# Performance work log

Hardware: AMD Instinct MI355X
Metric: run time of the kernel (lower is better)

The kernel has to match this reference:

```python
import jax, jax.numpy as jnp
import numpy as np


def _conv1x1(x, w, b):
    # x: (B, C, H, W), w: (O, C), b: (O,) -> (B, O, H, W)
    return jnp.einsum('bchw,oc->bohw', x, w) + b[None, :, None, None]


def setup_inputs() -> dict:
    key = jax.random.key(0)
    ks = jax.random.split(key, 9)
    C, Cb = 256, 128
    B, H, W = 4, 64, 64
    s_in = 1.0 / np.sqrt(C)   # kaiming-uniform-ish scale for 1x1 convs
    s_bn = 1.0 / np.sqrt(Cb)
    return {
        'x': jax.random.normal(ks[0], (B, C, H, W), dtype=jnp.float32),
        'theta_w': jax.random.uniform(ks[1], (Cb, C), jnp.float32, -s_in, s_in),
        'theta_b': jax.random.uniform(ks[2], (Cb,), jnp.float32, -s_in, s_in),
        'phi_w': jax.random.uniform(ks[3], (Cb, C), jnp.float32, -s_in, s_in),
        'phi_b': jax.random.uniform(ks[4], (Cb,), jnp.float32, -s_in, s_in),
        'g_w': jax.random.uniform(ks[5], (Cb, C), jnp.float32, -s_in, s_in),
        'g_b': jax.random.uniform(ks[6], (Cb,), jnp.float32, -s_in, s_in),
        'W_w': jax.random.uniform(ks[7], (C, Cb), jnp.float32, -s_bn, s_bn),
        'W_b': jax.random.uniform(ks[8], (C,), jnp.float32, -s_bn, s_bn),
    }


def reference(x, theta_w, theta_b, phi_w, phi_b, g_w, g_b, W_w, W_b):
    B, C, H, Wd = x.shape
    Cb = theta_w.shape[0]
    # NOTE: the original uses raw torch.reshape (row-major), NOT transpose,
    # so (B, Cb, H, W) -> (B, H*W, Cb) scrambles channel/spatial layout.
    # We replicate that exactly with jnp.reshape.
    theta = _conv1x1(x, theta_w, theta_b).reshape(B, -1, Cb)   # (B, N, Cb)
    phi = _conv1x1(x, phi_w, phi_b).reshape(B, Cb, -1)         # (B, Cb, N)
    g = _conv1x1(x, g_w, g_b).reshape(B, -1, Cb)               # (B, N, Cb)
    scores = jnp.einsum('bnc,bcm->bnm', theta, phi)            # (B, N, N)
    attn = jax.nn.softmax(scores, axis=1)                      # softmax over dim=1 (unusual axis)
    y = jnp.einsum('bnm,bmc->bnc', attn, g)                    # (B, N, Cb)
    y = y.reshape(B, -1, H, Wd)                                # raw reshape back to (B, Cb, H, W)
    w = _conv1x1(y, W_w, W_b)                                  # (B, C, H, W)
    return w + x
```

## Files before the change

### kernel.cpp

```cpp
#include <hip/hip_runtime.h>
#include <math.h>


constexpr int CI = 256;
constexpr int CB = 128;
constexpr int HWD = 4096;
constexpr int NBATCH = 4;
constexpr int NN_ = 4096;
constexpr size_t U1 = (size_t)NBATCH * NN_ * CB;
constexpr size_t U_THETA = 0;
constexpr size_t U_PHIT  = U1;
constexpr size_t U_G     = 2 * U1;
constexpr size_t U_GT    = 3 * U1;
constexpr size_t U_Y     = 4 * U1;
constexpr size_t U_XT    = 4 * U1;
constexpr size_t U_WCAT  = 8 * U1;
constexpr size_t U_WW    = 8 * U1 + 98304;
constexpr size_t F_D     = (8 * U1 + 131072) / 2;

typedef short v8s __attribute__((ext_vector_type(8)));
typedef unsigned short u8s __attribute__((ext_vector_type(8)));
typedef float v4f __attribute__((ext_vector_type(4)));
#define MFMA16(a, b, c) __builtin_amdgcn_mfma_f32_16x16x32_bf16(a, b, c, 0, 0, 0)

__device__ __forceinline__ unsigned short f2bf(float f) {
    union { float f; unsigned u; } v; v.f = f;
    unsigned r = v.u + 0x7fff + ((v.u >> 16) & 1);
    return (unsigned short)(r >> 16);
}
__device__ __forceinline__ float bf2f(unsigned short s) {
    union { unsigned u; float f; } v; v.u = (unsigned)s << 16;
    return v.f;
}

__global__ __launch_bounds__(256) void k0_xpose(
    const float* __restrict__ x, unsigned short* __restrict__ xT)
{
    __shared__ unsigned short T[64 * 72];
    const int t = threadIdx.x;
    const int hw0 = blockIdx.x * 64, c0 = blockIdx.y * 64, b = blockIdx.z;
    const float* xb = x + (size_t)b * CI * HWD;
    const int rr = t >> 4, cc = t & 15;
    #pragma unroll
    for (int pass = 0; pass < 4; pass++) {
        float4 f = *(const float4*)&xb[(size_t)(c0 + pass * 16 + rr) * HWD + hw0 + cc * 4];
        T[(cc * 4 + 0) * 72 + pass * 16 + rr] = f2bf(f.x);
        T[(cc * 4 + 1) * 72 + pass * 16 + rr] = f2bf(f.y);
        T[(cc * 4 + 2) * 72 + pass * 16 + rr] = f2bf(f.z);
        T[(cc * 4 + 3) * 72 + pass * 16 + rr] = f2bf(f.w);
    }
    __syncthreads();
    const int row = t >> 2, cs = (t & 3) * 16;
    unsigned short* dst = xT + (size_t)b * NN_ * CI;
    #pragma unroll
    for (int h = 0; h < 2; h++)
        *(u8s*)&dst[(size_t)(hw0 + row) * CI + c0 + cs + h * 8] =
            *(const u8s*)&T[row * 72 + cs + h * 8];
}

__global__ __launch_bounds__(256) void k0_weights(
    const float* __restrict__ tw, const float* __restrict__ pw,
    const float* __restrict__ gw, const float* __restrict__ Ww,
    unsigned short* __restrict__ wcat, unsigned short* __restrict__ wwB)
{
    int e = (blockIdx.x * 256 + threadIdx.x) * 4;
    const float* src; unsigned short* dst;
    if (e < 32768)       { src = tw + e;          dst = wcat + e; }
    else if (e < 65536)  { src = pw + (e - 32768); dst = wcat + e; }
    else if (e < 98304)  { src = gw + (e - 65536); dst = wcat + e; }
    else                 { src = Ww + (e - 98304); dst = wwB + (e - 98304); }
    float4 f = *(const float4*)src;
    ushort4 u;
    u.x = f2bf(f.x); u.y = f2bf(f.y); u.z = f2bf(f.z); u.w = f2bf(f.w);
    *(ushort4*)dst = u;
}

__global__ __launch_bounds__(256, 2) void k1_mfma(
    const unsigned short* __restrict__ xT, const unsigned short* __restrict__ wcat,
    const float* __restrict__ tb, const float* __restrict__ pb,
    const float* __restrict__ gb,
    unsigned short* __restrict__ thetaB, unsigned short* __restrict__ phiTB,
    unsigned short* __restrict__ gB)
{
    __shared__ unsigned short T[64 * 72];
    const int t = threadIdx.x;
    const int lane = t & 63, w = t >> 6;
    const int ln = lane & 15, quad = lane >> 4;
    const int hw0 = blockIdx.x * 64, j0 = blockIdx.y * 64, b = blockIdx.z;
    const int matId = j0 >> 7, jl0 = j0 & 127;
    const float* bvec = (matId == 0) ? tb : (matId == 1) ? pb : gb;
    const unsigned short* xb = xT + (size_t)b * NN_ * CI;

    v8s aw[8];
    #pragma unroll
    for (int kt = 0; kt < 8; kt++)
        aw[kt] = *(const v8s*)&wcat[(size_t)(j0 + w * 16 + ln) * CI + kt * 32 + quad * 8];

    v4f s[4] = {};
    v8s bx[4], bxn[4];
    #pragma unroll
    for (int mt = 0; mt < 4; mt++)
        bx[mt] = *(const v8s*)&xb[(size_t)(hw0 + mt * 16 + ln) * CI + quad * 8];
    #pragma unroll
    for (int kt = 0; kt < 8; kt++) {
        if (kt < 7) {
            #pragma unroll
            for (int mt = 0; mt < 4; mt++)
                bxn[mt] = *(const v8s*)&xb[(size_t)(hw0 + mt * 16 + ln) * CI + (kt + 1) * 32 + quad * 8];
        }
        #pragma unroll
        for (int mt = 0; mt < 4; mt++)
            s[mt] = MFMA16(aw[kt], bx[mt], s[mt]);
        #pragma unroll
        for (int mt = 0; mt < 4; mt++) bx[mt] = bxn[mt];
    }

    float bias[4];
    #pragma unroll
    for (int r = 0; r < 4; r++) bias[r] = bvec[jl0 + w * 16 + quad * 4 + r];

    if (matId != 1) {
        unsigned short* dst = ((matId == 0) ? thetaB : gB) + (size_t)b * CB * HWD;
        #pragma unroll
        for (int mt = 0; mt < 4; mt++)
            #pragma unroll
            for (int r = 0; r < 4; r++)
                dst[(size_t)(jl0 + w * 16 + quad * 4 + r) * HWD + hw0 + mt * 16 + ln] =
                    f2bf(s[mt][r] + bias[r]);
    } else {
        #pragma unroll
        for (int mt = 0; mt < 4; mt++) {
            ushort4 pk;
            pk.x = f2bf(s[mt][0] + bias[0]);
            pk.y = f2bf(s[mt][1] + bias[1]);
            pk.z = f2bf(s[mt][2] + bias[2]);
            pk.w = f2bf(s[mt][3] + bias[3]);
            *(ushort4*)&T[(mt * 16 + ln) * 72 + w * 16 + quad * 4] = pk;
        }
        __syncthreads();
        unsigned short* dst = phiTB + (size_t)b * NN_ * CB;
        const int row = t >> 2, cs = (t & 3) * 16;
        #pragma unroll
        for (int h = 0; h < 2; h++)
            *(u8s*)&dst[(size_t)(hw0 + row) * CB + jl0 + cs + h * 8] =
                *(const u8s*)&T[row * 72 + cs + h * 8];
    }
}

__global__ __launch_bounds__(256, 4) void k2_colsum(
    const unsigned short* __restrict__ thetaB,
    const unsigned short* __restrict__ phiTB,
    float* __restrict__ Dout)
{
    __shared__ float part[4][64];
    const int t = threadIdx.x;
    const int lane = t & 63, w = t >> 6;
    const int ln = lane & 15, quad = lane >> 4;
    const int m0 = blockIdx.x * 64, q = blockIdx.y, b = blockIdx.z;
    const unsigned short* th = thetaB + (size_t)b * NN_ * CB;
    const unsigned short* ph = phiTB + (size_t)b * NN_ * CB;

    v8s bf[4][4];
    #pragma unroll
    for (int mt = 0; mt < 4; mt++)
        #pragma unroll
        for (int kt = 0; kt < 4; kt++)
            bf[mt][kt] = *(const v8s*)&ph[(size_t)(m0 + mt * 16 + ln) * CB + kt * 32 + quad * 8];

    float dsum[4] = {0.f, 0.f, 0.f, 0.f};
    const int nBeg = q * 1024 + w * 16, nEnd = q * 1024 + 1024;
    v8s af[4], afn[4];
    #pragma unroll
    for (int kt = 0; kt < 4; kt++)
        af[kt] = *(const v8s*)&th[(size_t)(nBeg + ln) * CB + kt * 32 + quad * 8];
    for (int n0 = nBeg; n0 < nEnd; n0 += 64) {
        int nn = (n0 + 64 < nEnd) ? n0 + 64 : nBeg;
        #pragma unroll
        for (int kt = 0; kt < 4; kt++)
            afn[kt] = *(const v8s*)&th[(size_t)(nn + ln) * CB + kt * 32 + quad * 8];
        v4f s[4] = {};
        #pragma unroll
        for (int mt = 0; mt < 4; mt++)
            #pragma unroll
            for (int kt = 0; kt < 4; kt++)
                s[mt] = MFMA16(af[kt], bf[mt][kt], s[mt]);
        #pragma unroll
        for (int mt = 0; mt < 4; mt++)
            #pragma unroll
            for (int r = 0; r < 4; r++)
                dsum[mt] += __expf(s[mt][r]);
        #pragma unroll
        for (int kt = 0; kt < 4; kt++) af[kt] = afn[kt];
    }
    #pragma unroll
    for (int mt = 0; mt < 4; mt++) {
        float v = dsum[mt];
        v += __shfl_xor(v, 16);
        v += __shfl_xor(v, 32);
        dsum[mt] = v;
    }
    if (quad == 0) {
        #pragma unroll
        for (int mt = 0; mt < 4; mt++) part[w][mt * 16 + ln] = dsum[mt];
    }
    __syncthreads();
    if (t < 64) {
        float v = part[0][t] + part[1][t] + part[2][t] + part[3][t];
        Dout[((size_t)q * NBATCH + b) * NN_ + m0 + t] = v;
    }
}

__global__ __launch_bounds__(256) void k1b_transpose_scale_g(
    const unsigned short* __restrict__ gB, const float* __restrict__ D,
    unsigned short* __restrict__ gTB)
{
    const int t = threadIdx.x;
    const int m0 = blockIdx.x * 32;
    const int c0 = blockIdx.y * 64;
    const int b  = blockIdx.z;
    const unsigned short* src = gB + (size_t)b * CB * HWD;
    unsigned short* dst = gTB + (size_t)b * CB * HWD;
    const int c = c0 + (t & 63);
    const int mseg = (t >> 6) * 8;
    u8s pack;
    #pragma unroll
    for (int j = 0; j < 8; j++) {
        int m = m0 + mseg + j;
        float d = D[((size_t)0 * NBATCH + b) * NN_ + m]
                + D[((size_t)1 * NBATCH + b) * NN_ + m]
                + D[((size_t)2 * NBATCH + b) * NN_ + m]
                + D[((size_t)3 * NBATCH + b) * NN_ + m];
        float r = 1.0f / d;
        pack[j] = f2bf(bf2f(src[(size_t)m * CB + c]) * r);
    }
    *(u8s*)&dst[(size_t)c * HWD + m0 + mseg] = pack;
}

__global__ __launch_bounds__(256, 4) void k3_attn(
    const unsigned short* __restrict__ thetaB,
    const unsigned short* __restrict__ phiTB,
    const unsigned short* __restrict__ gTB,
    unsigned short* __restrict__ Y)
{
    __shared__ unsigned short Lphi[64 * 136];
    __shared__ unsigned short Pl[64][72];
    const int t = threadIdx.x;
    const int lane = t & 63, w = t >> 6;
    const int ln = lane & 15, quad = lane >> 4;
    const int rowS = t >> 4, colS = t & 15;
    const int n0 = blockIdx.x * 64, q = blockIdx.y, b = blockIdx.z;
    const unsigned short* th = thetaB + (size_t)b * NN_ * CB;
    const unsigned short* ph = phiTB + (size_t)b * NN_ * CB;
    const unsigned short* gT = gTB + (size_t)b * CB * HWD;

    v8s ath[4];
    #pragma unroll
    for (int kt = 0; kt < 4; kt++)
        ath[kt] = *(const v8s*)&th[(size_t)(n0 + w * 16 + ln) * CB + kt * 32 + quad * 8];

    const int mBeg = q * 1024, mEnd = mBeg + 1024;
    #pragma unroll
    for (int pass = 0; pass < 4; pass++) {
        v8s v = *(const v8s*)&ph[(size_t)(mBeg + pass * 16 + rowS) * CB + colS * 8];
        *(v8s*)&Lphi[(pass * 16 + rowS) * 136 + colS * 8] = v;
    }
    __syncthreads();

    v4f yacc[2][4] = {};
    for (int m0 = mBeg; m0 < mEnd; m0 += 64) {
        int mN = (m0 + 64 < mEnd) ? m0 + 64 : mBeg;
        v8s preg[4];
        #pragma unroll
        for (int pass = 0; pass < 4; pass++)
            preg[pass] = *(const v8s*)&ph[(size_t)(mN + pass * 16 + rowS) * CB + colS * 8];
        v8s gfrag[2][2];
        #pragma unroll
        for (int ct = 0; ct < 2; ct++)
            #pragma unroll
            for (int kt2 = 0; kt2 < 2; kt2++)
                gfrag[ct][kt2] = *(const v8s*)&gT[(size_t)(w * 32 + ct * 16 + ln) * HWD + m0 + kt2 * 32 + quad * 8];
        v4f s[4] = {};
        #pragma unroll
        for (int mt = 0; mt < 4; mt++)
            #pragma unroll
            for (int kt = 0; kt < 4; kt++) {
                v8s bphi = *(const v8s*)&Lphi[(mt * 16 + ln) * 136 + kt * 32 + quad * 8];
                s[mt] = MFMA16(ath[kt], bphi, s[mt]);
            }
        float pv[4][4];
        #pragma unroll
        for (int mt = 0; mt < 4; mt++)
            #pragma unroll
            for (int r = 0; r < 4; r++)
                pv[mt][r] = __expf(s[mt][r]);
        __syncthreads();
        #pragma unroll
        for (int mt = 0; mt < 4; mt++)
            #pragma unroll
            for (int r = 0; r < 4; r++)
                Pl[w * 16 + quad * 4 + r][mt * 16 + ln] = f2bf(pv[mt][r]);
        #pragma unroll
        for (int pass = 0; pass < 4; pass++)
            *(v8s*)&Lphi[(pass * 16 + rowS) * 136 + colS * 8] = preg[pass];
        __syncthreads();
        #pragma unroll
        for (int ct = 0; ct < 2; ct++)
            #pragma unroll
            for (int kt2 = 0; kt2 < 2; kt2++)
                #pragma unroll
                for (int nt = 0; nt < 4; nt++) {
                    v8s ap = *(const v8s*)&Pl[nt * 16 + ln][kt2 * 32 + quad * 8];
                    yacc[ct][nt] = MFMA16(ap, gfrag[ct][kt2], yacc[ct][nt]);
                }
    }
    unsigned short* yp = Y + ((size_t)q * NBATCH + b) * CB * HWD;
    #pragma unroll
    for (int ct = 0; ct < 2; ct++)
        #pragma unroll
        for (int nt = 0; nt < 4; nt++)
            #pragma unroll
            for (int r = 0; r < 4; r++)
                yp[(size_t)(n0 + nt * 16 + quad * 4 + r) * CB + w * 32 + ct * 16 + ln] =
                    f2bf(yacc[ct][nt][r]);
}

__global__ __launch_bounds__(256, 2) void k4_mfma(
    const float* __restrict__ x, const unsigned short* __restrict__ wwB,
    const float* __restrict__ Wb, const unsigned short* __restrict__ Ybuf,
    float* __restrict__ out)
{
    __shared__ unsigned short Yt[64 * 136];
    const int t = threadIdx.x;
    const int lane = t & 63, w = t >> 6;
    const int ln = lane & 15, quad = lane >> 4;
    const int hw0 = blockIdx.x * 64, o0 = blockIdx.y * 128, b = blockIdx.z;

    const int cb = t >> 1, seg = (t & 1) * 32;
    #pragma unroll
    for (int g8 = 0; g8 < 4; g8++) {
        float sum[8] = {};
        #pragma unroll
        for (int q = 0; q < 4; q++) {
            u8s u = *(const u8s*)&Ybuf[((size_t)q * NBATCH + b) * CB * HWD +
                                       (size_t)cb * HWD + hw0 + seg + g8 * 8];
            #pragma unroll
            for (int j = 0; j < 8; j++) sum[j] += bf2f(u[j]);
        }
        #pragma unroll
        for (int j = 0; j < 8; j++)
            Yt[(seg + g8 * 8 + j) * 136 + cb] = f2bf(sum[j]);
    }
    __syncthreads();

    v8s aw[2][4];
    #pragma unroll
    for (int os = 0; os < 2; os++)
        #pragma unroll
        for (int kt = 0; kt < 4; kt++)
            aw[os][kt] = *(const v8s*)&wwB[(size_t)(o0 + w * 32 + os * 16 + ln) * CB + kt * 32 + quad * 8];

    v4f s[2][4] = {};
    #pragma unroll
    for (int kt = 0; kt < 4; kt++) {
        v8s by[4];
        #pragma unroll
        for (int mt = 0; mt < 4; mt++)
            by[mt] = *(const v8s*)&Yt[(mt * 16 + ln) * 136 + kt * 32 + quad * 8];
        #pragma unroll
        for (int os = 0; os < 2; os++)
            #pragma unroll
            for (int mt = 0; mt < 4; mt++)
                s[os][mt] = MFMA16(aw[os][kt], by[mt], s[os][mt]);
    }
    float bias[2][4];
    #pragma unroll
    for (int os = 0; os < 2; os++)
        #pragma unroll
        for (int r = 0; r < 4; r++)
            bias[os][r] = Wb[o0 + w * 32 + os * 16 + quad * 4 + r];
    #pragma unroll
    for (int os = 0; os < 2; os++)
        #pragma unroll
        for (int mt = 0; mt < 4; mt++)
            #pragma unroll
            for (int r = 0; r < 4; r++) {
                int o = o0 + w * 32 + os * 16 + quad * 4 + r;
                size_t idx = (size_t)b * CI * HWD + (size_t)o * HWD + hw0 + mt * 16 + ln;
                out[idx] = s[os][mt][r] + bias[os][r] + x[idx];
            }
}

extern "C" void kernel_launch(void* const* d_in, const int* in_sizes, int n_in,
                              void* d_out, int out_size, void* d_ws, size_t ws_size,
                              hipStream_t stream)
{
    const float* x  = (const float*)d_in[0];
    const float* tw = (const float*)d_in[1];
    const float* tb = (const float*)d_in[2];
    const float* pw = (const float*)d_in[3];
    const float* pb = (const float*)d_in[4];
    const float* gw = (const float*)d_in[5];
    const float* gb = (const float*)d_in[6];
    const float* Ww = (const float*)d_in[7];
    const float* Wb = (const float*)d_in[8];
    unsigned short* wsu = (unsigned short*)d_ws;
    float* wsf = (float*)d_ws;
    unsigned short* thetaB = wsu + U_THETA;
    unsigned short* phiTB  = wsu + U_PHIT;
    unsigned short* gB     = wsu + U_G;
    unsigned short* gTB    = wsu + U_GT;
    unsigned short* Ybuf   = wsu + U_Y;
    unsigned short* xTB    = wsu + U_XT;
    unsigned short* wcatB  = wsu + U_WCAT;
    unsigned short* wwB    = wsu + U_WW;
    float* Dbuf = wsf + F_D;
    float* out = (float*)d_out;
    dim3 blk(256, 1, 1);
    hipLaunchKernelGGL(k0_xpose, dim3(64, 4, NBATCH), blk, 0, stream, x, xTB);
    hipLaunchKernelGGL(k0_weights, dim3(128, 1, 1), blk, 0, stream,
                       tw, pw, gw, Ww, wcatB, wwB);
    hipLaunchKernelGGL(k1_mfma, dim3(64, 6, NBATCH), blk, 0, stream,
                       xTB, wcatB, tb, pb, gb, thetaB, phiTB, gB);
    hipLaunchKernelGGL(k2_colsum, dim3(64, 4, NBATCH), blk, 0, stream,
                       thetaB, phiTB, Dbuf);
    hipLaunchKernelGGL(k1b_transpose_scale_g, dim3(128, 2, NBATCH), blk, 0, stream,
                       gB, Dbuf, gTB);
    hipLaunchKernelGGL(k3_attn, dim3(64, 4, NBATCH), blk, 0, stream,
                       thetaB, phiTB, gTB, Ybuf);
    hipLaunchKernelGGL(k4_mfma, dim3(64, 2, NBATCH), blk, 0, stream,
                       x, wwB, Wb, Ybuf, out);
}
```

Before: 215.0 us.

## Switch projection and attention kernels to 32x32 MFMA and LDS-staged transposes

Replaces the 16x16x32 bf16 MFMA tiling in the projection and attention kernels with 32x32x16 MFMA tiles. Each wave now computes a 32x32 output block, which cuts fragment loads per FLOP. The projection kernel stages the x tile in LDS and raises occupancy to 4 blocks per CU. The g transpose-and-scale kernel is rewritten to do vector reads and write through an LDS transpose, and the padded LDS strides are changed. Risks include new bank conflicts from the scalar LDS scatter writes and more register pressure from the 16-float accumulators.

```diff
diff --git a/kernel.cpp b/kernel.cpp
--- a/kernel.cpp
+++ b/kernel.cpp
@@ -1,6 +1,5 @@
 #include <hip/hip_runtime.h>
 #include <math.h>
-
 
 constexpr int CI = 256;
 constexpr int CB = 128;
@@ -21,7 +20,9 @@
 typedef short v8s __attribute__((ext_vector_type(8)));
 typedef unsigned short u8s __attribute__((ext_vector_type(8)));
 typedef float v4f __attribute__((ext_vector_type(4)));
+typedef float v16f __attribute__((ext_vector_type(16)));
 #define MFMA16(a, b, c) __builtin_amdgcn_mfma_f32_16x16x32_bf16(a, b, c, 0, 0, 0)
+#define MFMA32(a, b, c) __builtin_amdgcn_mfma_f32_32x32x16_bf16(a, b, c, 0, 0, 0)
 
 __device__ __forceinline__ unsigned short f2bf(float f) {
     union { float f; unsigned u; } v; v.f = f;
@@ -75,67 +76,56 @@
     *(ushort4*)dst = u;
 }
 
-__global__ __launch_bounds__(256, 2) void k1_mfma(
+__global__ __launch_bounds__(256, 4) void k1_mfma(
     const unsigned short* __restrict__ xT, const unsigned short* __restrict__ wcat,
     const float* __restrict__ tb, const float* __restrict__ pb,
     const float* __restrict__ gb,
     unsigned short* __restrict__ thetaB, unsigned short* __restrict__ phiTB,
     unsigned short* __restrict__ gB)
 {
-    __shared__ unsigned short T[64 * 72];
+    __shared__ unsigned short LdsX[64 * 268];
+    unsigned short* T = LdsX;
     const int t = threadIdx.x;
     const int lane = t & 63, w = t >> 6;
-    const int ln = lane & 15, quad = lane >> 4;
+    const int l31 = lane & 31, lh = lane >> 5;
+    const int qj = w >> 1, qh = w & 1;
     const int hw0 = blockIdx.x * 64, j0 = blockIdx.y * 64, b = blockIdx.z;
     const int matId = j0 >> 7, jl0 = j0 & 127;
     const float* bvec = (matId == 0) ? tb : (matId == 1) ? pb : gb;
     const unsigned short* xb = xT + (size_t)b * NN_ * CI;
 
-    v8s aw[8];
-    #pragma unroll
-    for (int kt = 0; kt < 8; kt++)
-        aw[kt] = *(const v8s*)&wcat[(size_t)(j0 + w * 16 + ln) * CI + kt * 32 + quad * 8];
-
-    v4f s[4] = {};
-    v8s bx[4], bxn[4];
-    #pragma unroll
-    for (int mt = 0; mt < 4; mt++)
-        bx[mt] = *(const v8s*)&xb[(size_t)(hw0 + mt * 16 + ln) * CI + quad * 8];
-    #pragma unroll
-    for (int kt = 0; kt < 8; kt++) {
-        if (kt < 7) {
-            #pragma unroll
-            for (int mt = 0; mt < 4; mt++)
-                bxn[mt] = *(const v8s*)&xb[(size_t)(hw0 + mt * 16 + ln) * CI + (kt + 1) * 32 + quad * 8];
-        }
-        #pragma unroll
-        for (int mt = 0; mt < 4; mt++)
-            s[mt] = MFMA16(aw[kt], bx[mt], s[mt]);
-        #pragma unroll
-        for (int mt = 0; mt < 4; mt++) bx[mt] = bxn[mt];
-    }
-
-    float bias[4];
-    #pragma unroll
-    for (int r = 0; r < 4; r++) bias[r] = bvec[jl0 + w * 16 + quad * 4 + r];
+    {
+        const int row = t >> 2, seg = t & 3;
+        #pragma unroll
+        for (int c8 = 0; c8 < 8; c8++)
+            *(u8s*)&LdsX[row * 268 + seg * 64 + c8 * 8] =
+                *(const u8s*)&xb[(size_t)(hw0 + row) * CI + seg * 64 + c8 * 8];
+    }
+    __syncthreads();
+
+    v16f s = {};
+    #pragma unroll
+    for (int kt = 0; kt < 16; kt++) {
+        v8s a = *(const v8s*)&wcat[(size_t)(j0 + qj * 32 + l31) * CI + kt * 16 + lh * 8];
+        v8s bx = *(const v8s*)&LdsX[(qh * 32 + l31) * 268 + kt * 16 + lh * 8];
+        s = MFMA32(a, bx, s);
+    }
 
     if (matId != 1) {
         unsigned short* dst = ((matId == 0) ? thetaB : gB) + (size_t)b * CB * HWD;
         #pragma unroll
-        for (int mt = 0; mt < 4; mt++)
-            #pragma unroll
-            for (int r = 0; r < 4; r++)
-                dst[(size_t)(jl0 + w * 16 + quad * 4 + r) * HWD + hw0 + mt * 16 + ln] =
-                    f2bf(s[mt][r] + bias[r]);
+        for (int reg = 0; reg < 16; reg++) {
+            int row = (reg & 3) + 8 * (reg >> 2) + 4 * lh;
+            int cb = jl0 + qj * 32 + row;
+            dst[(size_t)cb * HWD + hw0 + qh * 32 + l31] = f2bf(s[reg] + bvec[cb]);
+        }
     } else {
-        #pragma unroll
-        for (int mt = 0; mt < 4; mt++) {
-            ushort4 pk;
-            pk.x = f2bf(s[mt][0] + bias[0]);
-            pk.y = f2bf(s[mt][1] + bias[1]);
-            pk.z = f2bf(s[mt][2] + bias[2]);
-            pk.w = f2bf(s[mt][3] + bias[3]);
-            *(ushort4*)&T[(mt * 16 + ln) * 72 + w * 16 + quad * 4] = pk;
+        __syncthreads();
+        #pragma unroll
+        for (int reg = 0; reg < 16; reg++) {
+            int row = (reg & 3) + 8 * (reg >> 2) + 4 * lh;
+            T[(qh * 32 + l31) * 76 + qj * 32 + row] =
+                f2bf(s[reg] + bvec[jl0 + qj * 32 + row]);
         }
         __syncthreads();
         unsigned short* dst = phiTB + (size_t)b * NN_ * CB;
@@ -143,7 +133,7 @@
         #pragma unroll
         for (int h = 0; h < 2; h++)
             *(u8s*)&dst[(size_t)(hw0 + row) * CB + jl0 + cs + h * 8] =
-                *(const u8s*)&T[row * 72 + cs + h * 8];
+                *(const u8s*)&T[row * 76 + cs + h * 8];
     }
 }
 
@@ -214,26 +204,35 @@
     const unsigned short* __restrict__ gB, const float* __restrict__ D,
     unsigned short* __restrict__ gTB)
 {
+    __shared__ unsigned short T[128 * 36];
     const int t = threadIdx.x;
     const int m0 = blockIdx.x * 32;
-    const int c0 = blockIdx.y * 64;
     const int b  = blockIdx.z;
-    const unsigned short* src = gB + (size_t)b * CB * HWD;
+    const unsigned short* F = gB + (size_t)b * CB * HWD;
     unsigned short* dst = gTB + (size_t)b * CB * HWD;
-    const int c = c0 + (t & 63);
-    const int mseg = (t >> 6) * 8;
-    u8s pack;
-    #pragma unroll
-    for (int j = 0; j < 8; j++) {
-        int m = m0 + mseg + j;
+    const int mrow = t >> 3, cg = t & 7;
+    {
+        int m = m0 + mrow;
         float d = D[((size_t)0 * NBATCH + b) * NN_ + m]
                 + D[((size_t)1 * NBATCH + b) * NN_ + m]
                 + D[((size_t)2 * NBATCH + b) * NN_ + m]
                 + D[((size_t)3 * NBATCH + b) * NN_ + m];
         float r = 1.0f / d;
-        pack[j] = f2bf(bf2f(src[(size_t)m * CB + c]) * r);
-    }
-    *(u8s*)&dst[(size_t)c * HWD + m0 + mseg] = pack;
+        #pragma unroll
+        for (int j8 = 0; j8 < 2; j8++) {
+            int cbase = cg * 8 + j8 * 64;
+            u8s u = *(const u8s*)&F[(size_t)m * CB + cbase];
+            #pragma unroll
+            for (int e = 0; e < 8; e++)
+                T[(cbase + e) * 36 + mrow] = f2bf(bf2f(u[e]) * r);
+        }
+    }
+    __syncthreads();
+    const int c = t >> 1, mh = (t & 1) * 16;
+    #pragma unroll
+    for (int h8 = 0; h8 < 2; h8++)
+        *(u8s*)&dst[(size_t)c * HWD + m0 + mh + h8 * 8] =
+            *(const u8s*)&T[c * 36 + mh + h8 * 8];
 }
 
 __global__ __launch_bounds__(256, 4) void k3_attn(
@@ -242,86 +241,71 @@
     const unsigned short* __restrict__ gTB,
     unsigned short* __restrict__ Y)
 {
-    __shared__ unsigned short Lphi[64 * 136];
-    __shared__ unsigned short Pl[64][72];
+    __shared__ unsigned short Lphi[64 * 140];
+    __shared__ unsigned short Pl[64 * 76];
     const int t = threadIdx.x;
     const int lane = t & 63, w = t >> 6;
-    const int ln = lane & 15, quad = lane >> 4;
+    const int l31 = lane & 31, lh = lane >> 5;
+    const int qn = w & 1, qm = w >> 1;
     const int rowS = t >> 4, colS = t & 15;
     const int n0 = blockIdx.x * 64, q = blockIdx.y, b = blockIdx.z;
     const unsigned short* th = thetaB + (size_t)b * NN_ * CB;
     const unsigned short* ph = phiTB + (size_t)b * NN_ * CB;
     const unsigned short* gT = gTB + (size_t)b * CB * HWD;
 
-    v8s ath[4];
-    #pragma unroll
-    for (int kt = 0; kt < 4; kt++)
-        ath[kt] = *(const v8s*)&th[(size_t)(n0 + w * 16 + ln) * CB + kt * 32 + quad * 8];
+    v8s ath[8];
+    #pragma unroll
+    for (int kt = 0; kt < 8; kt++)
+        ath[kt] = *(const v8s*)&th[(size_t)(n0 + qn * 32 + l31) * CB + kt * 16 + lh * 8];
 
     const int mBeg = q * 1024, mEnd = mBeg + 1024;
     #pragma unroll
-    for (int pass = 0; pass < 4; pass++) {
-        v8s v = *(const v8s*)&ph[(size_t)(mBeg + pass * 16 + rowS) * CB + colS * 8];
-        *(v8s*)&Lphi[(pass * 16 + rowS) * 136 + colS * 8] = v;
-    }
-    __syncthreads();
-
-    v4f yacc[2][4] = {};
+    for (int pass = 0; pass < 4; pass++)
+        *(v8s*)&Lphi[(pass * 16 + rowS) * 140 + colS * 8] =
+            *(const v8s*)&ph[(size_t)(mBeg + pass * 16 + rowS) * CB + colS * 8];
+    __syncthreads();
+
+    v16f yacc[2] = {};
     for (int m0 = mBeg; m0 < mEnd; m0 += 64) {
         int mN = (m0 + 64 < mEnd) ? m0 + 64 : mBeg;
         v8s preg[4];
         #pragma unroll
         for (int pass = 0; pass < 4; pass++)
             preg[pass] = *(const v8s*)&ph[(size_t)(mN + pass * 16 + rowS) * CB + colS * 8];
-        v8s gfrag[2][2];
-        #pragma unroll
-        for (int ct = 0; ct < 2; ct++)
-            #pragma unroll
-            for (int kt2 = 0; kt2 < 2; kt2++)
-                gfrag[ct][kt2] = *(const v8s*)&gT[(size_t)(w * 32 + ct * 16 + ln) * HWD + m0 + kt2 * 32 + quad * 8];
-        v4f s[4] = {};
-        #pragma unroll
-        for (int mt = 0; mt < 4; mt++)
-            #pragma unroll
-            for (int kt = 0; kt < 4; kt++) {
-                v8s bphi = *(const v8s*)&Lphi[(mt * 16 + ln) * 136 + kt * 32 + quad * 8];
-                s[mt] = MFMA16(ath[kt], bphi, s[mt]);
+        v16f s = {};
+        #pragma unroll
+        for (int kt = 0; kt < 8; kt++) {
+            v8s bphi = *(const v8s*)&Lphi[(qm * 32 + l31) * 140 + kt * 16 + lh * 8];
+            s = MFMA32(ath[kt], bphi, s);
+        }
+        __syncthreads();
+        #pragma unroll
+        for (int reg = 0; reg < 16; reg++) {
+            int row = qn * 32 + (reg & 3) + 8 * (reg >> 2) + 4 * lh;
+            Pl[row * 76 + qm * 32 + l31] = f2bf(__expf(s[reg]));
+        }
+        #pragma unroll
+        for (int pass = 0; pass < 4; pass++)
+            *(v8s*)&Lphi[(pass * 16 + rowS) * 140 + colS * 8] = preg[pass];
+        __syncthreads();
+        #pragma unroll
+        for (int kstep = 0; kstep < 4; kstep++) {
+            v8s bg = *(const v8s*)&gT[(size_t)(w * 32 + l31) * HWD + m0 + kstep * 16 + lh * 8];
+            #pragma unroll
+            for (int nt = 0; nt < 2; nt++) {
+                v8s ap = *(const v8s*)&Pl[(nt * 32 + l31) * 76 + kstep * 16 + lh * 8];
+                yacc[nt] = MFMA32(ap, bg, yacc[nt]);
             }
-        float pv[4][4];
-        #pragma unroll
-        for (int mt = 0; mt < 4; mt++)
-            #pragma unroll
-            for (int r = 0; r < 4; r++)
-                pv[mt][r] = __expf(s[mt][r]);
-        __syncthreads();
-        #pragma unroll
-        for (int mt = 0; mt < 4; mt++)
-            #pragma unroll
-            for (int r = 0; r < 4; r++)
-                Pl[w * 16 + quad * 4 + r][mt * 16 + ln] = f2bf(pv[mt][r]);
-        #pragma unroll
-        for (int pass = 0; pass < 4; pass++)
-            *(v8s*)&Lphi[(pass * 16 + rowS) * 136 + colS * 8] = preg[pass];
-        __syncthreads();
-        #pragma unroll
-        for (int ct = 0; ct < 2; ct++)
-            #pragma unroll
-            for (int kt2 = 0; kt2 < 2; kt2++)
-                #pragma unroll
-                for (int nt = 0; nt < 4; nt++) {
-                    v8s ap = *(const v8s*)&Pl[nt * 16 + ln][kt2 * 32 + quad * 8];
-                    yacc[ct][nt] = MFMA16(ap, gfrag[ct][kt2], yacc[ct][nt]);
-                }
+        }
     }
     unsigned short* yp = Y + ((size_t)q * NBATCH + b) * CB * HWD;
     #pragma unroll
-    for (int ct = 0; ct < 2; ct++)
-        #pragma unroll
-        for (int nt = 0; nt < 4; nt++)
-            #pragma unroll
-            for (int r = 0; r < 4; r++)
-                yp[(size_t)(n0 + nt * 16 + quad * 4 + r) * CB + w * 32 + ct * 16 + ln] =
-                    f2bf(yacc[ct][nt][r]);
+    for (int nt = 0; nt < 2; nt++)
+        #pragma unroll
+        for (int reg = 0; reg < 16; reg++) {
+            int row = (reg & 3) + 8 * (reg >> 2) + 4 * lh;
+            yp[(size_t)(n0 + nt * 32 + row) * CB + w * 32 + l31] = f2bf(yacc[nt][reg]);
+        }
 }
 
 __global__ __launch_bounds__(256, 2) void k4_mfma(
@@ -372,12 +356,6 @@
             for (int mt = 0; mt < 4; mt++)
                 s[os][mt] = MFMA16(aw[os][kt], by[mt], s[os][mt]);
     }
-    float bias[2][4];
-    #pragma unroll
-    for (int os = 0; os < 2; os++)
-        #pragma unroll
-        for (int r = 0; r < 4; r++)
-            bias[os][r] = Wb[o0 + w * 32 + os * 16 + quad * 4 + r];
     #pragma unroll
     for (int os = 0; os < 2; os++)
         #pragma unroll
@@ -386,7 +364,7 @@
             for (int r = 0; r < 4; r++) {
                 int o = o0 + w * 32 + os * 16 + quad * 4 + r;
                 size_t idx = (size_t)b * CI * HWD + (size_t)o * HWD + hw0 + mt * 16 + ln;
-                out[idx] = s[os][mt][r] + bias[os][r] + x[idx];
+                out[idx] = s[os][mt][r] + Wb[o] + x[idx];
             }
 }
 
@@ -423,7 +401,7 @@
                        xTB, wcatB, tb, pb, gb, thetaB, phiTB, gB);
     hipLaunchKernelGGL(k2_colsum, dim3(64, 4, NBATCH), blk, 0, stream,
                        thetaB, phiTB, Dbuf);
-    hipLaunchKernelGGL(k1b_transpose_scale_g, dim3(128, 2, NBATCH), blk, 0, stream,
+    hipLaunchKernelGGL(k1b_transpose_scale_g, dim3(128, 1, NBATCH), blk, 0, stream,
                        gB, Dbuf, gTB);
     hipLaunchKernelGGL(k3_attn, dim3(64, 4, NBATCH), blk, 0, stream,
                        thetaB, phiTB, gTB, Ybuf);
```

New measurement: 211.0 us. Within noise of the previous version (-1.8%).
